# Optimization experiments

Hardware: AMD Instinct MI355X
Metric: run time of the kernel (lower is better)

Reference implementation:

```python
import jax, jax.numpy as jnp
import numpy as np

B, H, W = 64, 512, 512          # batch, image height/width
BH, BW = 8, 8                   # block_size
K = 256                         # n_blocks (codebook size)
L = BH * BW                     # block_len = 64
HT, WT = H // BH, W // BW       # tiles per axis
T = HT * WT                     # tiles_per_img = 4096
BETA = 35.0


def _unfold(img):
    # img: (B, 1, H, W) -> patches (B, T, L), matching torch.nn.Unfold
    # with kernel=stride=(BH,BW): tiles row-major, patch flattened (kh, kw).
    x = img.reshape(B, 1, HT, BH, WT, BW)
    x = x.transpose(0, 2, 4, 1, 3, 5)          # (B, HT, WT, 1, BH, BW)
    return x.reshape(B, T, L)


def _fold(patches):
    # patches: (B, T, L) -> img (B, 1, H, W); exact inverse of _unfold
    # (non-overlapping, so Fold is pure reassembly, no accumulation).
    x = patches.reshape(B, HT, WT, 1, BH, BW)
    x = x.transpose(0, 3, 1, 4, 2, 5)          # (B, 1, HT, BH, WT, BW)
    return x.reshape(B, 1, H, W)


def setup_inputs() -> dict:
    key = jax.random.key(0)
    k1, k2 = jax.random.split(key)
    target_img = jax.random.uniform(k1, (B, 1, H, W), dtype=jnp.float32)
    # Learned codebook parameter (Haar-ish init in the original; values
    # don't change the math being tested).
    blocks = jax.random.uniform(k2, (K, BH, BW), dtype=jnp.float32)
    return {"target_img": target_img, "blocks": blocks}


def reference(target_img, blocks):
    patches = _unfold(target_img).reshape(B * T, L)   # (N, L), N = B*T
    codes = blocks.reshape(K, L)                      # (K, L)

    # Squared distances ||a - b||^2 via the expanded form to avoid
    # materializing the (N, K, L) difference tensor.
    a2 = jnp.sum(patches * patches, axis=-1, keepdims=True)   # (N, 1)
    b2 = jnp.sum(codes * codes, axis=-1)                      # (K,)
    ab = patches @ codes.T                                    # (N, K)
    sqerr = a2 - 2.0 * ab + b2                                # (N, K)

    block_weights = jax.nn.softmax(-BETA * sqerr, axis=-1)    # (N, K)
    uf_reconstructed = block_weights @ codes                  # (N, L)

    reconstructed = _fold(uf_reconstructed.reshape(B, T, L))  # (B,1,H,W)
    choice_penalty = jnp.mean(
        jnp.minimum(block_weights, 1.0 - block_weights)) * K
    return reconstructed, choice_penalty
```

## Files before the change

### kernel.cpp

```cpp
#include <hip/hip_runtime.h>
#include <hip/hip_fp16.h>


typedef short short8 __attribute__((ext_vector_type(8)));
typedef float floatx4 __attribute__((ext_vector_type(4)));

namespace {
constexpr float BETA_C = 35.0f;
constexpr float TAU    = 1e-6f;
constexpr float INV_N  = 1.0f / 262144.0f;
constexpr size_t IMG_ELEMS = (size_t)64 * 512 * 512;
constexpr int WB   = 0;
constexpr int WA_H = 9216;
constexpr int WA_L = 11264;
constexpr int WW   = 0;
constexpr int WR   = 8448;
constexpr int NWORDS = 13312;
}

__device__ __forceinline__ unsigned short f2bf(float x) {
  unsigned u = __float_as_uint(x);
  return (unsigned short)((u + 0x7FFFu + ((u >> 16) & 1u)) >> 16);
}
__device__ __forceinline__ float bf2f(unsigned short h) {
  return __uint_as_float((unsigned)h << 16);
}
__device__ __forceinline__ unsigned pack2(unsigned short lo, unsigned short hi) {
  return (unsigned)lo | ((unsigned)hi << 16);
}

__global__ void pack_codes(const float* __restrict__ blk,
                           unsigned* __restrict__ wsBh,
                           unsigned* __restrict__ wsBl,
                           float* __restrict__ wsB2) {
  const int c = threadIdx.x;
  const float* src = blk + c * 64;
  float b2 = 0.f;
#pragma unroll
  for (int g = 0; g < 8; ++g) {
#pragma unroll
    for (int t = 0; t < 4; ++t) {
      float v0 = src[g * 8 + 2 * t], v1 = src[g * 8 + 2 * t + 1];
      b2 += v0 * v0 + v1 * v1;
      unsigned short h0 = f2bf(v0), h1 = f2bf(v1);
      unsigned short l0 = f2bf(v0 - bf2f(h0)), l1 = f2bf(v1 - bf2f(h1));
      wsBh[(c * 8 + g) * 4 + t] = pack2(h0, h1);
      wsBl[(c * 8 + g) * 4 + t] = pack2(l0, l1);
    }
  }
  wsB2[c] = b2;
}

__global__ __launch_bounds__(256, 3) void recon_kernel(
    const float* __restrict__ img, const float* __restrict__ blk,
    const unsigned* __restrict__ wsBh, const unsigned* __restrict__ wsBl,
    const float* __restrict__ wsB2, float* __restrict__ out,
    float* __restrict__ penAcc) {
  __shared__ unsigned sMem[NWORDS];
  float* sMemF = reinterpret_cast<float*>(sMem);

  const int tid = threadIdx.x;
  const int lane = tid & 63;
  const int wave = tid >> 6;
  const int b = blockIdx.x >> 6;
  const int ht = blockIdx.x & 63;
  const int c15 = lane & 15;
  const int q = lane >> 4;

  {
    const uint4* src = reinterpret_cast<const uint4*>(wsBh);
#pragma unroll
    for (int i = 0; i < 8; ++i) {
      int j = i * 256 + tid;
      *reinterpret_cast<uint4*>(&sMem[WB + (j + (j >> 3)) * 4]) = src[j];
    }
  }
  const float* imgBase = img + (size_t)b * (512 * 512) + (size_t)(ht * 8) * 512;
#pragma unroll
  for (int i = 0; i < 4; ++i) {
    int f4 = i * 256 + tid;
    int row = f4 >> 7, c4 = f4 & 127;
    float4 v = reinterpret_cast<const float4*>(imgBase + row * 512)[c4];
    int wt = c4 >> 1, hw = c4 & 1;
    unsigned short h0 = f2bf(v.x), h1 = f2bf(v.y), h2 = f2bf(v.z), h3 = f2bf(v.w);
    unsigned short l0 = f2bf(v.x - bf2f(h0)), l1 = f2bf(v.y - bf2f(h1));
    unsigned short l2 = f2bf(v.z - bf2f(h2)), l3 = f2bf(v.w - bf2f(h3));
    int base = wt * 32 + row * 4 + hw * 2;
    *reinterpret_cast<uint2*>(&sMem[WA_H + base]) =
        make_uint2(pack2(h0, h1), pack2(h2, h3));
    *reinterpret_cast<uint2*>(&sMem[WA_L + base]) =
        make_uint2(pack2(l0, l1), pack2(l2, l3));
  }
  __syncthreads();

  const int patch = wave * 16 + c15;
  short8 ah[2], al[2];
#pragma unroll
  for (int s = 0; s < 2; ++s) {
    int base = patch * 32 + (4 * s + q) * 4;
    ah[s] = *reinterpret_cast<const short8*>(&sMem[WA_H + base]);
    al[s] = *reinterpret_cast<const short8*>(&sMem[WA_L + base]);
  }

  floatx4 acc[16];
#pragma unroll
  for (int n = 0; n < 16; ++n) acc[n] = (floatx4){0.f, 0.f, 0.f, 0.f};

#pragma unroll
  for (int n = 0; n < 16; ++n) {
    const unsigned* pb = &sMem[WB + (144 * n + 9 * c15 + q) * 4];
    short8 b0 = *reinterpret_cast<const short8*>(pb);
    short8 b1 = *reinterpret_cast<const short8*>(pb + 16);
    acc[n] = __builtin_amdgcn_mfma_f32_16x16x32_bf16(ah[0], b0, acc[n], 0, 0, 0);
    acc[n] = __builtin_amdgcn_mfma_f32_16x16x32_bf16(al[0], b0, acc[n], 0, 0, 0);
    acc[n] = __builtin_amdgcn_mfma_f32_16x16x32_bf16(ah[1], b1, acc[n], 0, 0, 0);
    acc[n] = __builtin_amdgcn_mfma_f32_16x16x32_bf16(al[1], b1, acc[n], 0, 0, 0);
  }
  __syncthreads();
  {
    const uint4* src = reinterpret_cast<const uint4*>(wsBl);
#pragma unroll
    for (int i = 0; i < 8; ++i) {
      int j = i * 256 + tid;
      *reinterpret_cast<uint4*>(&sMem[WB + (j + (j >> 3)) * 4]) = src[j];
    }
  }
  __syncthreads();
#pragma unroll
  for (int n = 0; n < 16; ++n) {
    const unsigned* pb = &sMem[WB + (144 * n + 9 * c15 + q) * 4];
    short8 b0 = *reinterpret_cast<const short8*>(pb);
    short8 b1 = *reinterpret_cast<const short8*>(pb + 16);
    acc[n] = __builtin_amdgcn_mfma_f32_16x16x32_bf16(ah[0], b0, acc[n], 0, 0, 0);
    acc[n] = __builtin_amdgcn_mfma_f32_16x16x32_bf16(al[0], b0, acc[n], 0, 0, 0);
    acc[n] = __builtin_amdgcn_mfma_f32_16x16x32_bf16(ah[1], b1, acc[n], 0, 0, 0);
    acc[n] = __builtin_amdgcn_mfma_f32_16x16x32_bf16(al[1], b1, acc[n], 0, 0, 0);
  }

#pragma unroll
  for (int n = 0; n < 16; ++n) {
    float b2v = wsB2[16 * n + c15];
#pragma unroll
    for (int r = 0; r < 4; ++r)
      acc[n][r] = fmaf(2.0f * BETA_C, acc[n][r], -BETA_C * b2v);
  }
  float mx[4], sm[4];
#pragma unroll
  for (int r = 0; r < 4; ++r) {
    float m = acc[0][r];
#pragma unroll
    for (int n = 1; n < 16; ++n) m = fmaxf(m, acc[n][r]);
#pragma unroll
    for (int off = 1; off <= 8; off <<= 1) m = fmaxf(m, __shfl_xor(m, off, 64));
    mx[r] = m;
    sm[r] = 0.f;
  }
#pragma unroll
  for (int n = 0; n < 16; ++n)
#pragma unroll
    for (int r = 0; r < 4; ++r) {
      acc[n][r] = __expf(acc[n][r] - mx[r]);
      sm[r] += acc[n][r];
    }
#pragma unroll
  for (int r = 0; r < 4; ++r) {
#pragma unroll
    for (int off = 1; off <= 8; off <<= 1) sm[r] += __shfl_xor(sm[r], off, 64);
    sm[r] = 1.0f / sm[r];
  }

  __syncthreads();

  float pen = 0.f;
#pragma unroll
  for (int n = 0; n < 16; ++n)
#pragma unroll
    for (int r = 0; r < 4; ++r) {
      float w = acc[n][r] * sm[r];
      pen += fminf(w, 1.0f - w);
      float wp = __shfl_xor(w, 1, 64);
      if (!(c15 & 1)) {
        int p = wave * 16 + 4 * q + r;
        sMem[WW + p * 132 + 8 * n + (c15 >> 1)] = pack2(f2bf(w), f2bf(wp));
      }
    }
#pragma unroll
  for (int off = 1; off <= 32; off <<= 1) pen += __shfl_xor(pen, off, 64);
  if (lane == 0) atomicAdd(penAcc, pen);

#pragma unroll 1
  for (int pl = 0; pl < 16; ++pl) {
    int p = wave * 16 + pl;
    unsigned u0 = sMem[WW + p * 132 + lane];
    unsigned u1 = sMem[WW + p * 132 + 64 + lane];
    float w0 = bf2f((unsigned short)(u0 & 0xFFFFu));
    float w1 = bf2f((unsigned short)(u0 >> 16));
    float w2 = bf2f((unsigned short)(u1 & 0xFFFFu));
    float w3 = bf2f((unsigned short)(u1 >> 16));
    bool flag = (w0 > TAU) || (w1 > TAU) || (w2 > TAU) || (w3 > TAU);
    unsigned long long msk = __ballot(flag);
    float rr = 0.f;
    while (msk) {
      int L = __builtin_ctzll(msk);
      msk &= msk - 1;
      unsigned a0 = (unsigned)__shfl((int)u0, L, 64);
      unsigned a1 = (unsigned)__shfl((int)u1, L, 64);
      float p0 = bf2f((unsigned short)(a0 & 0xFFFFu));
      float p1 = bf2f((unsigned short)(a0 >> 16));
      float p2 = bf2f((unsigned short)(a1 & 0xFFFFu));
      float p3 = bf2f((unsigned short)(a1 >> 16));
      const float* cb = blk + 2 * L * 64 + lane;
      if (p0 > TAU) rr = fmaf(p0, cb[0], rr);
      if (p1 > TAU) rr = fmaf(p1, cb[64], rr);
      if (p2 > TAU) rr = fmaf(p2, cb[128 * 64], rr);
      if (p3 > TAU) rr = fmaf(p3, cb[128 * 64 + 64], rr);
    }
    sMemF[WR + p * 68 + lane] = rr;
  }
  __syncthreads();

  float* outBase = out + (size_t)b * (512 * 512) + (size_t)(ht * 8) * 512;
#pragma unroll
  for (int i = 0; i < 4; ++i) {
    int f4 = i * 256 + tid;
    int row = f4 >> 7, c4 = f4 & 127;
    int wt = c4 >> 1, hw = c4 & 1;
    float4 v = *reinterpret_cast<const float4*>(
        &sMemF[WR + wt * 68 + row * 8 + hw * 4]);
    reinterpret_cast<float4*>(outBase + row * 512)[c4] = v;
  }
}

__global__ void finalize_kernel(float* penSlot) {
  *penSlot = (*penSlot) * INV_N;
}

extern "C" void kernel_launch(void* const* d_in, const int* in_sizes, int n_in,
                              void* d_out, int out_size, void* d_ws, size_t ws_size,
                              hipStream_t stream) {
  const float* img = (const float*)d_in[0];
  const float* blk = (const float*)d_in[1];
  float* out = (float*)d_out;
  float* penSlot = out + IMG_ELEMS;

  unsigned* wsBh = (unsigned*)d_ws;
  unsigned* wsBl = wsBh + 8192;
  float* wsB2 = (float*)(wsBl + 8192);

  pack_codes<<<dim3(1), dim3(256), 0, stream>>>(blk, wsBh, wsBl, wsB2);
  hipMemsetAsync(penSlot, 0, sizeof(float), stream);
  recon_kernel<<<dim3(4096), dim3(256), 0, stream>>>(img, blk, wsBh, wsBl,
                                                     wsB2, out, penSlot);
  finalize_kernel<<<dim3(1), dim3(1), 0, stream>>>(penSlot);
}
```

Baseline: 360.2 us.

## Load A fragments directly to registers, XOR-swizzle codebook LDS, fuse weight-gather reconstruction

Each lane now loads its image patch fragment straight from global memory into registers and converts it to bf16 hi/lo there, so the LDS staging of A and one barrier go away. The codebook copy in LDS switches from padded rows to an XOR swizzle, shrinking shared memory and raising launch bounds to 4 blocks per CU. The reconstruction skips the packed bf16 weight round-trip through LDS: weights stay in fp32 registers and a per-row ballot/readlane loop accumulates into per-patch registers. The cost is more ballot loop iterations, divergent switch code and more register pressure, which may fight the higher occupancy target.

Result: faster. 328.4 us (-8.8%).

```diff
diff --git a/kernel.cpp b/kernel.cpp
--- a/kernel.cpp
+++ b/kernel.cpp
@@ -1,5 +1,4 @@
 #include <hip/hip_runtime.h>
-#include <hip/hip_fp16.h>
 
 
 typedef short short8 __attribute__((ext_vector_type(8)));
@@ -10,12 +9,9 @@
 constexpr float TAU    = 1e-6f;
 constexpr float INV_N  = 1.0f / 262144.0f;
 constexpr size_t IMG_ELEMS = (size_t)64 * 512 * 512;
-constexpr int WB   = 0;
-constexpr int WA_H = 9216;
-constexpr int WA_L = 11264;
-constexpr int WW   = 0;
-constexpr int WR   = 8448;
-constexpr int NWORDS = 13312;
+constexpr int WB = 0;
+constexpr int WR = 0;
+constexpr int NWORDS = 8192;
 }
 
 __device__ __forceinline__ unsigned short f2bf(float x) {
@@ -27,6 +23,15 @@
 }
 __device__ __forceinline__ unsigned pack2(unsigned short lo, unsigned short hi) {
   return (unsigned)lo | ((unsigned)hi << 16);
+}
+__device__ __forceinline__ void cvt8(float4 a, float4 b, short8& h, short8& l) {
+  float f[8] = {a.x, a.y, a.z, a.w, b.x, b.y, b.z, b.w};
+#pragma unroll
+  for (int i = 0; i < 8; ++i) {
+    unsigned short hh = f2bf(f[i]);
+    h[i] = (short)hh;
+    l[i] = (short)f2bf(f[i] - bf2f(hh));
+  }
 }
 
 __global__ void pack_codes(const float* __restrict__ blk,
@@ -51,7 +56,7 @@
   wsB2[c] = b2;
 }
 
-__global__ __launch_bounds__(256, 3) void recon_kernel(
+__global__ __launch_bounds__(256, 4) void recon_kernel(
     const float* __restrict__ img, const float* __restrict__ blk,
     const unsigned* __restrict__ wsBh, const unsigned* __restrict__ wsBl,
     const float* __restrict__ wsB2, float* __restrict__ out,
@@ -67,50 +72,40 @@
   const int c15 = lane & 15;
   const int q = lane >> 4;
 
+  const float* imgBase = img + (size_t)b * (512 * 512) + (size_t)(ht * 8) * 512;
+  const float* aptr = imgBase + q * 512 + (wave * 16 + c15) * 8;
+  float4 v00 = *reinterpret_cast<const float4*>(aptr);
+  float4 v01 = *reinterpret_cast<const float4*>(aptr + 4);
+  float4 v10 = *reinterpret_cast<const float4*>(aptr + 2048);
+  float4 v11 = *reinterpret_cast<const float4*>(aptr + 2048 + 4);
+
   {
     const uint4* src = reinterpret_cast<const uint4*>(wsBh);
 #pragma unroll
     for (int i = 0; i < 8; ++i) {
       int j = i * 256 + tid;
-      *reinterpret_cast<uint4*>(&sMem[WB + (j + (j >> 3)) * 4]) = src[j];
-    }
-  }
-  const float* imgBase = img + (size_t)b * (512 * 512) + (size_t)(ht * 8) * 512;
-#pragma unroll
-  for (int i = 0; i < 4; ++i) {
-    int f4 = i * 256 + tid;
-    int row = f4 >> 7, c4 = f4 & 127;
-    float4 v = reinterpret_cast<const float4*>(imgBase + row * 512)[c4];
-    int wt = c4 >> 1, hw = c4 & 1;
-    unsigned short h0 = f2bf(v.x), h1 = f2bf(v.y), h2 = f2bf(v.z), h3 = f2bf(v.w);
-    unsigned short l0 = f2bf(v.x - bf2f(h0)), l1 = f2bf(v.y - bf2f(h1));
-    unsigned short l2 = f2bf(v.z - bf2f(h2)), l3 = f2bf(v.w - bf2f(h3));
-    int base = wt * 32 + row * 4 + hw * 2;
-    *reinterpret_cast<uint2*>(&sMem[WA_H + base]) =
-        make_uint2(pack2(h0, h1), pack2(h2, h3));
-    *reinterpret_cast<uint2*>(&sMem[WA_L + base]) =
-        make_uint2(pack2(l0, l1), pack2(l2, l3));
-  }
-  __syncthreads();
-
-  const int patch = wave * 16 + c15;
+      int sj = (j & ~7) | ((j ^ (j >> 3)) & 7);
+      *reinterpret_cast<uint4*>(&sMem[WB + j * 4]) = src[sj];
+    }
+  }
+
   short8 ah[2], al[2];
-#pragma unroll
-  for (int s = 0; s < 2; ++s) {
-    int base = patch * 32 + (4 * s + q) * 4;
-    ah[s] = *reinterpret_cast<const short8*>(&sMem[WA_H + base]);
-    al[s] = *reinterpret_cast<const short8*>(&sMem[WA_L + base]);
-  }
+  cvt8(v00, v01, ah[0], al[0]);
+  cvt8(v10, v11, ah[1], al[1]);
+  __syncthreads();
 
   floatx4 acc[16];
 #pragma unroll
   for (int n = 0; n < 16; ++n) acc[n] = (floatx4){0.f, 0.f, 0.f, 0.f};
 
+  const int kx = c15 & 7;
+  const unsigned* pb0 = &sMem[WB + (8 * c15 + (q ^ kx)) * 4];
+  const unsigned* pb1 = &sMem[WB + (8 * c15 + ((q ^ 4) ^ kx)) * 4];
+
 #pragma unroll
   for (int n = 0; n < 16; ++n) {
-    const unsigned* pb = &sMem[WB + (144 * n + 9 * c15 + q) * 4];
-    short8 b0 = *reinterpret_cast<const short8*>(pb);
-    short8 b1 = *reinterpret_cast<const short8*>(pb + 16);
+    short8 b0 = *reinterpret_cast<const short8*>(pb0 + 512 * n);
+    short8 b1 = *reinterpret_cast<const short8*>(pb1 + 512 * n);
     acc[n] = __builtin_amdgcn_mfma_f32_16x16x32_bf16(ah[0], b0, acc[n], 0, 0, 0);
     acc[n] = __builtin_amdgcn_mfma_f32_16x16x32_bf16(al[0], b0, acc[n], 0, 0, 0);
     acc[n] = __builtin_amdgcn_mfma_f32_16x16x32_bf16(ah[1], b1, acc[n], 0, 0, 0);
@@ -122,15 +117,15 @@
 #pragma unroll
     for (int i = 0; i < 8; ++i) {
       int j = i * 256 + tid;
-      *reinterpret_cast<uint4*>(&sMem[WB + (j + (j >> 3)) * 4]) = src[j];
+      int sj = (j & ~7) | ((j ^ (j >> 3)) & 7);
+      *reinterpret_cast<uint4*>(&sMem[WB + j * 4]) = src[sj];
     }
   }
   __syncthreads();
 #pragma unroll
   for (int n = 0; n < 16; ++n) {
-    const unsigned* pb = &sMem[WB + (144 * n + 9 * c15 + q) * 4];
-    short8 b0 = *reinterpret_cast<const short8*>(pb);
-    short8 b1 = *reinterpret_cast<const short8*>(pb + 16);
+    short8 b0 = *reinterpret_cast<const short8*>(pb0 + 512 * n);
+    short8 b1 = *reinterpret_cast<const short8*>(pb1 + 512 * n);
     acc[n] = __builtin_amdgcn_mfma_f32_16x16x32_bf16(ah[0], b0, acc[n], 0, 0, 0);
     acc[n] = __builtin_amdgcn_mfma_f32_16x16x32_bf16(al[0], b0, acc[n], 0, 0, 0);
     acc[n] = __builtin_amdgcn_mfma_f32_16x16x32_bf16(ah[1], b1, acc[n], 0, 0, 0);
@@ -169,65 +164,51 @@
     sm[r] = 1.0f / sm[r];
   }
 
-  __syncthreads();
-
   float pen = 0.f;
-#pragma unroll
-  for (int n = 0; n < 16; ++n)
-#pragma unroll
-    for (int r = 0; r < 4; ++r) {
+  float rr[16] = {0.f, 0.f, 0.f, 0.f, 0.f, 0.f, 0.f, 0.f,
+                  0.f, 0.f, 0.f, 0.f, 0.f, 0.f, 0.f, 0.f};
+#pragma unroll
+  for (int r = 0; r < 4; ++r) {
+#pragma unroll
+    for (int n = 0; n < 16; ++n) {
       float w = acc[n][r] * sm[r];
       pen += fminf(w, 1.0f - w);
-      float wp = __shfl_xor(w, 1, 64);
-      if (!(c15 & 1)) {
-        int p = wave * 16 + 4 * q + r;
-        sMem[WW + p * 132 + 8 * n + (c15 >> 1)] = pack2(f2bf(w), f2bf(wp));
+      unsigned long long m = __ballot(w > TAU);
+      while (m) {
+        int L = __builtin_ctzll(m);
+        m &= m - 1;
+        float wL = __uint_as_float(
+            __builtin_amdgcn_readlane(__float_as_uint(w), L));
+        float v = wL * blk[(16 * n + (L & 15)) * 64 + lane];
+        switch (L >> 4) {
+          case 0: rr[r] += v; break;
+          case 1: rr[4 + r] += v; break;
+          case 2: rr[8 + r] += v; break;
+          case 3: rr[12 + r] += v; break;
+        }
       }
     }
+  }
 #pragma unroll
   for (int off = 1; off <= 32; off <<= 1) pen += __shfl_xor(pen, off, 64);
   if (lane == 0) atomicAdd(penAcc, pen);
 
-#pragma unroll 1
-  for (int pl = 0; pl < 16; ++pl) {
-    int p = wave * 16 + pl;
-    unsigned u0 = sMem[WW + p * 132 + lane];
-    unsigned u1 = sMem[WW + p * 132 + 64 + lane];
-    float w0 = bf2f((unsigned short)(u0 & 0xFFFFu));
-    float w1 = bf2f((unsigned short)(u0 >> 16));
-    float w2 = bf2f((unsigned short)(u1 & 0xFFFFu));
-    float w3 = bf2f((unsigned short)(u1 >> 16));
-    bool flag = (w0 > TAU) || (w1 > TAU) || (w2 > TAU) || (w3 > TAU);
-    unsigned long long msk = __ballot(flag);
-    float rr = 0.f;
-    while (msk) {
-      int L = __builtin_ctzll(msk);
-      msk &= msk - 1;
-      unsigned a0 = (unsigned)__shfl((int)u0, L, 64);
-      unsigned a1 = (unsigned)__shfl((int)u1, L, 64);
-      float p0 = bf2f((unsigned short)(a0 & 0xFFFFu));
-      float p1 = bf2f((unsigned short)(a0 >> 16));
-      float p2 = bf2f((unsigned short)(a1 & 0xFFFFu));
-      float p3 = bf2f((unsigned short)(a1 >> 16));
-      const float* cb = blk + 2 * L * 64 + lane;
-      if (p0 > TAU) rr = fmaf(p0, cb[0], rr);
-      if (p1 > TAU) rr = fmaf(p1, cb[64], rr);
-      if (p2 > TAU) rr = fmaf(p2, cb[128 * 64], rr);
-      if (p3 > TAU) rr = fmaf(p3, cb[128 * 64 + 64], rr);
-    }
-    sMemF[WR + p * 68 + lane] = rr;
-  }
-  __syncthreads();
-
-  float* outBase = out + (size_t)b * (512 * 512) + (size_t)(ht * 8) * 512;
+  __syncthreads();
+
+#pragma unroll
+  for (int pl = 0; pl < 16; ++pl)
+    sMemF[WR + (wave * 16 + pl) * 68 + lane] = rr[pl];
+  float* outBase = out + (size_t)b * (512 * 512) + (size_t)(ht * 8) * 512 +
+                   wave * 128;
 #pragma unroll
   for (int i = 0; i < 4; ++i) {
-    int f4 = i * 256 + tid;
-    int row = f4 >> 7, c4 = f4 & 127;
-    int wt = c4 >> 1, hw = c4 & 1;
+    int f = i * 64 + lane;
+    int row = f >> 5;
+    int cc = f & 31;
+    int wtl = cc >> 1, hw = cc & 1;
     float4 v = *reinterpret_cast<const float4*>(
-        &sMemF[WR + wt * 68 + row * 8 + hw * 4]);
-    reinterpret_cast<float4*>(outBase + row * 512)[c4] = v;
+        &sMemF[WR + (wave * 16 + wtl) * 68 + row * 8 + hw * 4]);
+    *reinterpret_cast<float4*>(outBase + row * 512 + cc * 4) = v;
   }
 }
 
```
